# Performance work log

Hardware: AMD Instinct MI355X
Metric: run time of the kernel (lower is better)

Reference implementation:

```python
import jax, jax.numpy as jnp
import numpy as np

NEG_SLOPE = 0.2  # PyG GATConv default negative_slope
EPS = 1e-16      # PyG softmax denominator epsilon


def gat_conv(x, src, dst, W, b, att_src, att_dst, num_nodes):
    """PyG GATConv, heads=1, add_self_loops=True (self loops already in src/dst).
    x: [N, Fin]; src/dst: [E]; W: [Fin, Fout]; att_src/att_dst: [Fout]."""
    h = x @ W                                  # [N, Fout]
    a_src = h @ att_src                        # [N]
    a_dst = h @ att_dst                        # [N]
    e = jax.nn.leaky_relu(a_src[src] + a_dst[dst], NEG_SLOPE)  # [E]
    m = jax.ops.segment_max(e, dst, num_segments=num_nodes)    # softmax over edges grouped by dst
    ex = jnp.exp(e - m[dst])
    denom = jax.ops.segment_sum(ex, dst, num_segments=num_nodes)
    alpha = ex / (denom[dst] + EPS)            # [E]
    out = jax.ops.segment_sum(alpha[:, None] * h[src], dst, num_segments=num_nodes)
    return out + b


def global_attention(x, gate_w, gate_b):
    """PyG GlobalAttention with a single graph: softmax(gate_nn(x)) weighted sum."""
    gate = x @ gate_w + gate_b                 # [N, 1]
    attn = jax.nn.softmax(gate, axis=0)        # softmax over all nodes (one graph)
    return jnp.sum(attn * x, axis=0, keepdims=True)  # [1, F]


def setup_inputs() -> dict:
    key = jax.random.key(0)
    ks = jax.random.split(key, 12)
    N, E, D, H = 50000, 800000, 768, 256
    x = jax.random.normal(ks[0], (N, D), dtype=jnp.float32)
    edge_index = jax.random.randint(ks[1], (2, E), 0, N, dtype=jnp.int64)
    s = 1.0 / np.sqrt(D)
    W1 = jax.random.normal(ks[2], (D, H), dtype=jnp.float32) * s
    b1 = jnp.zeros((H,), dtype=jnp.float32)
    as1 = jax.random.normal(ks[3], (H,), dtype=jnp.float32) * (1.0 / np.sqrt(H))
    ad1 = jax.random.normal(ks[4], (H,), dtype=jnp.float32) * (1.0 / np.sqrt(H))
    s2 = 1.0 / np.sqrt(H)
    W2 = jax.random.normal(ks[5], (H, H), dtype=jnp.float32) * s2
    b2 = jnp.zeros((H,), dtype=jnp.float32)
    as2 = jax.random.normal(ks[6], (H,), dtype=jnp.float32) * s2
    ad2 = jax.random.normal(ks[7], (H,), dtype=jnp.float32) * s2
    gate_w = jax.random.normal(ks[8], (H, 1), dtype=jnp.float32) * s2
    gate_b = jnp.zeros((1,), dtype=jnp.float32)
    return {"x": x, "edge_index": edge_index, "W1": W1, "b1": b1, "as1": as1,
            "ad1": ad1, "W2": W2, "b2": b2, "as2": as2, "ad2": ad2,
            "gate_w": gate_w, "gate_b": gate_b}


def reference(x, edge_index, W1, b1, as1, ad1, W2, b2, as2, ad2, gate_w, gate_b):
    N = x.shape[0]
    loops = jnp.arange(N, dtype=edge_index.dtype)
    src = jnp.concatenate([edge_index[0], loops])  # add self loops (GATConv default)
    dst = jnp.concatenate([edge_index[1], loops])
    h = gat_conv(x, src, dst, W1, b1, as1, ad1, N)
    h = jax.nn.relu(h)
    h = gat_conv(h, src, dst, W2, b2, as2, ad2, N)
    h = jax.nn.relu(h)
    return global_attention(h, gate_w, gate_b)   # [1, 256]
```

## Files before the change

### kernel.cpp

```cpp
#include <hip/hip_runtime.h>

#define WAVE 64
#define LRELU(x) ((x) > 0.0f ? (x) : 0.2f * (x))

typedef __attribute__((ext_vector_type(8))) short bf16x8;
typedef __attribute__((ext_vector_type(4))) float f32x4;

__device__ __forceinline__ void gld16(const void* g, void* l) {
    __builtin_amdgcn_global_load_lds((const __attribute__((address_space(1))) unsigned int*)g,
                                     (__attribute__((address_space(3))) unsigned int*)l,
                                     16, 0, 0);
}

__device__ __forceinline__ unsigned short f2bf_hi(float f) {
    unsigned u = __builtin_bit_cast(unsigned, f);
    u += 0x7FFF + ((u >> 16) & 1);
    return (unsigned short)(u >> 16);
}

__device__ __forceinline__ float4 bf4_to_f32(ushort4 v) {
    float4 r;
    r.x = __builtin_bit_cast(float, (unsigned)v.x << 16);
    r.y = __builtin_bit_cast(float, (unsigned)v.y << 16);
    r.z = __builtin_bit_cast(float, (unsigned)v.z << 16);
    r.w = __builtin_bit_cast(float, (unsigned)v.w << 16);
    return r;
}

__device__ __forceinline__ void split8(f32x4 a, f32x4 b, bf16x8& hi, bf16x8& lo) {
    float f[8] = {a[0], a[1], a[2], a[3], b[0], b[1], b[2], b[3]};
#pragma unroll
    for (int e = 0; e < 8; e++) {
        unsigned u = __builtin_bit_cast(unsigned, f[e]);
        float hf = __builtin_bit_cast(float, u & 0xFFFF0000u);
        float fl = f[e] - hf;
        unsigned u2 = __builtin_bit_cast(unsigned, fl);
        unsigned t2 = u2 + 0x7FFF + ((u2 >> 16) & 1);
        hi[e] = (short)(u >> 16);
        lo[e] = (short)(t2 >> 16);
    }
}

__global__ __launch_bounds__(256) void k_gemm_f32A(const float* __restrict__ A,
                                                   const unsigned short* __restrict__ Bh,
                                                   const unsigned short* __restrict__ Bl,
                                                   unsigned short* __restrict__ Cb,
                                                   float* __restrict__ asrc,
                                                   float* __restrict__ adst,
                                                   const float* __restrict__ att_s,
                                                   const float* __restrict__ att_d,
                                                   int M, int K) {
    __shared__ char smem[32768];
    char* SAH = smem;
    char* SAL = smem + 8192;
    char* SBH = smem + 16384;
    char* SBL = smem + 24576;

    const int tid = threadIdx.x, lane = tid & 63, w = tid >> 6;
    const int m16 = lane & 15, q = lane >> 4;
    const int row0 = blockIdx.x * 128, col0 = blockIdx.y * 128;

    f32x4 acc[4][4];
#pragma unroll
    for (int i = 0; i < 4; i++)
#pragma unroll
        for (int j = 0; j < 4; j++) acc[i][j] = (f32x4){0.f, 0.f, 0.f, 0.f};

    const int s_row = tid >> 1;
    const int s_mt  = s_row >> 4, s_m16 = s_row & 15;
    const int s_q0  = (tid & 1) * 2;
    int s_grow = row0 + s_row;
    if (s_grow > M - 1) s_grow = M - 1;
    const f32x4* aptr = (const f32x4*)&A[(size_t)s_grow * K] + (tid & 1) * 4;
    const int s_off = (s_mt * 4 + s_q0) * 256 + s_m16 * 16;

    const int b_rloc = lane >> 2;
    const int b_kb   = (lane & 3) * 16;

    f32x4 pre0 = aptr[0], pre1 = aptr[1], pre2 = aptr[2], pre3 = aptr[3];

    for (int k0 = 0; k0 < K; k0 += 32) {
#pragma unroll
        for (int s = 0; s < 2; s++) {
            int c = w * 2 + s;
            int brow = col0 + c * 16 + b_rloc;
            gld16((const char*)Bh + ((size_t)brow * K + k0) * 2 + b_kb, SBH + c * 1024);
            gld16((const char*)Bl + ((size_t)brow * K + k0) * 2 + b_kb, SBL + c * 1024);
        }
        {
            bf16x8 h0, l0, h1, l1;
            split8(pre0, pre1, h0, l0);
            split8(pre2, pre3, h1, l1);
            *(bf16x8*)(SAH + s_off)       = h0;
            *(bf16x8*)(SAL + s_off)       = l0;
            *(bf16x8*)(SAH + s_off + 256) = h1;
            *(bf16x8*)(SAL + s_off + 256) = l1;
        }
        __syncthreads();

        if (k0 + 32 < K) {
            aptr += 8;
            pre0 = aptr[0]; pre1 = aptr[1]; pre2 = aptr[2]; pre3 = aptr[3];
        }

        bf16x8 bh[4], bl[4];
#pragma unroll
        for (int nt = 0; nt < 4; nt++) {
            int r = (w & 1) * 64 + nt * 16 + m16;
            bh[nt] = *(bf16x8*)(SBH + r * 64 + q * 16);
            bl[nt] = *(bf16x8*)(SBL + r * 64 + q * 16);
        }
#pragma unroll
        for (int mt = 0; mt < 4; mt++) {
            int frag = ((w >> 1) * 4 + mt) * 4 + q;
            bf16x8 ah = *(bf16x8*)(SAH + frag * 256 + m16 * 16);
            bf16x8 al = *(bf16x8*)(SAL + frag * 256 + m16 * 16);
#pragma unroll
            for (int nt = 0; nt < 4; nt++) {
                acc[mt][nt] = __builtin_amdgcn_mfma_f32_16x16x32_bf16(ah, bh[nt], acc[mt][nt], 0, 0, 0);
                acc[mt][nt] = __builtin_amdgcn_mfma_f32_16x16x32_bf16(ah, bl[nt], acc[mt][nt], 0, 0, 0);
                acc[mt][nt] = __builtin_amdgcn_mfma_f32_16x16x32_bf16(al, bh[nt], acc[mt][nt], 0, 0, 0);
            }
        }
        __syncthreads();
    }

    const int rbase = row0 + (w >> 1) * 64;
    const int cbase = col0 + (w & 1) * 64;
#pragma unroll
    for (int mt = 0; mt < 4; mt++)
#pragma unroll
        for (int r = 0; r < 4; r++) {
            int row = rbase + mt * 16 + q * 4 + r;
            if (row < M) {
#pragma unroll
                for (int nt = 0; nt < 4; nt++)
                    Cb[(size_t)row * 256 + cbase + nt * 16 + m16] = f2bf_hi(acc[mt][nt][r]);
            }
        }
    float as_v[4], ad_v[4];
#pragma unroll
    for (int nt = 0; nt < 4; nt++) {
        as_v[nt] = att_s[cbase + nt * 16 + m16];
        ad_v[nt] = att_d[cbase + nt * 16 + m16];
    }
#pragma unroll
    for (int mt = 0; mt < 4; mt++)
#pragma unroll
        for (int r = 0; r < 4; r++) {
            float s = 0.f, d = 0.f;
#pragma unroll
            for (int nt = 0; nt < 4; nt++) {
                float v = acc[mt][nt][r];
                s = fmaf(v, as_v[nt], s);
                d = fmaf(v, ad_v[nt], d);
            }
#pragma unroll
            for (int off = 1; off < 16; off <<= 1) {
                s += __shfl_xor(s, off);
                d += __shfl_xor(d, off);
            }
            int row = rbase + mt * 16 + q * 4 + r;
            if (m16 == 0 && row < M) {
                atomicAdd(&asrc[row], s);
                atomicAdd(&adst[row], d);
            }
        }
}

__global__ __launch_bounds__(256) void k_gemm_bf16A(const unsigned short* __restrict__ Ah,
                                                    const unsigned short* __restrict__ Al,
                                                    const unsigned short* __restrict__ Bh,
                                                    const unsigned short* __restrict__ Bl,
                                                    unsigned short* __restrict__ Cb,
                                                    float* __restrict__ asrc,
                                                    float* __restrict__ adst,
                                                    const float* __restrict__ att_s,
                                                    const float* __restrict__ att_d,
                                                    int M, int K) {
    __shared__ char smem[32768];
    char* SAH = smem;
    char* SAL = smem + 8192;
    char* SBH = smem + 16384;
    char* SBL = smem + 24576;

    const int tid = threadIdx.x, lane = tid & 63, w = tid >> 6;
    const int m16 = lane & 15, q = lane >> 4;
    const int row0 = blockIdx.x * 128, col0 = blockIdx.y * 128;

    f32x4 acc[4][4];
#pragma unroll
    for (int i = 0; i < 4; i++)
#pragma unroll
        for (int j = 0; j < 4; j++) acc[i][j] = (f32x4){0.f, 0.f, 0.f, 0.f};

    const int rloc = lane >> 2;
    const int kb   = (lane & 3) * 16;

    for (int k0 = 0; k0 < K; k0 += 32) {
#pragma unroll
        for (int s = 0; s < 2; s++) {
            int c = w * 2 + s;
            int arow = row0 + c * 16 + rloc;
            int brow = col0 + c * 16 + rloc;
            gld16((const char*)Ah + ((size_t)arow * K + k0) * 2 + kb, SAH + c * 1024);
            gld16((const char*)Al + ((size_t)arow * K + k0) * 2 + kb, SAL + c * 1024);
            gld16((const char*)Bh + ((size_t)brow * K + k0) * 2 + kb, SBH + c * 1024);
            gld16((const char*)Bl + ((size_t)brow * K + k0) * 2 + kb, SBL + c * 1024);
        }
        __syncthreads();

        bf16x8 bh[4], bl[4];
#pragma unroll
        for (int nt = 0; nt < 4; nt++) {
            int r = (w & 1) * 64 + nt * 16 + m16;
            bh[nt] = *(bf16x8*)(SBH + r * 64 + q * 16);
            bl[nt] = *(bf16x8*)(SBL + r * 64 + q * 16);
        }
#pragma unroll
        for (int mt = 0; mt < 4; mt++) {
            int r = (w >> 1) * 64 + mt * 16 + m16;
            bf16x8 ah = *(bf16x8*)(SAH + r * 64 + q * 16);
            bf16x8 al = *(bf16x8*)(SAL + r * 64 + q * 16);
#pragma unroll
            for (int nt = 0; nt < 4; nt++) {
                acc[mt][nt] = __builtin_amdgcn_mfma_f32_16x16x32_bf16(ah, bh[nt], acc[mt][nt], 0, 0, 0);
                acc[mt][nt] = __builtin_amdgcn_mfma_f32_16x16x32_bf16(ah, bl[nt], acc[mt][nt], 0, 0, 0);
                acc[mt][nt] = __builtin_amdgcn_mfma_f32_16x16x32_bf16(al, bh[nt], acc[mt][nt], 0, 0, 0);
            }
        }
        __syncthreads();
    }

    const int rbase = row0 + (w >> 1) * 64;
    const int cbase = col0 + (w & 1) * 64;
#pragma unroll
    for (int mt = 0; mt < 4; mt++)
#pragma unroll
        for (int r = 0; r < 4; r++) {
            int row = rbase + mt * 16 + q * 4 + r;
            if (row < M) {
#pragma unroll
                for (int nt = 0; nt < 4; nt++)
                    Cb[(size_t)row * 256 + cbase + nt * 16 + m16] = f2bf_hi(acc[mt][nt][r]);
            }
        }
    float as_v[4], ad_v[4];
#pragma unroll
    for (int nt = 0; nt < 4; nt++) {
        as_v[nt] = att_s[cbase + nt * 16 + m16];
        ad_v[nt] = att_d[cbase + nt * 16 + m16];
    }
#pragma unroll
    for (int mt = 0; mt < 4; mt++)
#pragma unroll
        for (int r = 0; r < 4; r++) {
            float s = 0.f, d = 0.f;
#pragma unroll
            for (int nt = 0; nt < 4; nt++) {
                float v = acc[mt][nt][r];
                s = fmaf(v, as_v[nt], s);
                d = fmaf(v, ad_v[nt], d);
            }
#pragma unroll
            for (int off = 1; off < 16; off <<= 1) {
                s += __shfl_xor(s, off);
                d += __shfl_xor(d, off);
            }
            int row = rbase + mt * 16 + q * 4 + r;
            if (m16 == 0 && row < M) {
                atomicAdd(&asrc[row], s);
                atomicAdd(&adst[row], d);
            }
        }
}

__global__ __launch_bounds__(256) void k_convB(const float* __restrict__ W,
                                               unsigned short* __restrict__ BThi,
                                               unsigned short* __restrict__ BTlo, int K) {
    int idx = blockIdx.x * 256 + threadIdx.x;
    int k = idx >> 8, n = idx & 255;
    if (k >= K) return;
    float f = W[(size_t)k * 256 + n];
    unsigned u = __builtin_bit_cast(unsigned, f);
    unsigned t = u + 0x7FFF + ((u >> 16) & 1);
    float hf = __builtin_bit_cast(float, t & 0xFFFF0000u);
    unsigned short lb = f2bf_hi(f - hf);
    BThi[(size_t)n * K + k] = (unsigned short)(t >> 16);
    BTlo[(size_t)n * K + k] = lb;
}

__global__ __launch_bounds__(256) void k_degree(const int* __restrict__ dst,
                                                int* __restrict__ counts, int E) {
    int e = blockIdx.x * 256 + threadIdx.x;
    if (e < E) atomicAdd(&counts[dst[e]], 1);
}

__global__ __launch_bounds__(256) void k_part(const int* __restrict__ counts,
                                              int* __restrict__ psum, int N) {
    __shared__ int red[256];
    int tid = threadIdx.x;
    int i = blockIdx.x * 256 + tid;
    red[tid] = (i < N) ? counts[i] : 0;
    __syncthreads();
    for (int off = 128; off; off >>= 1) {
        if (tid < off) red[tid] += red[tid + off];
        __syncthreads();
    }
    if (tid == 0) psum[blockIdx.x] = red[0];
}

__global__ __launch_bounds__(256) void k_scan_part(int* __restrict__ psum, int nb,
                                                   int* __restrict__ total_out) {
    __shared__ int s[256];
    int tid = threadIdx.x;
    int v = (tid < nb) ? psum[tid] : 0;
    s[tid] = v;
    __syncthreads();
    for (int off = 1; off < 256; off <<= 1) {
        int t = (tid >= off) ? s[tid - off] : 0;
        __syncthreads();
        s[tid] += t;
        __syncthreads();
    }
    if (tid < nb) psum[tid] = s[tid] - v;
    if (tid == 255) *total_out = s[255];
}

__global__ __launch_bounds__(256) void k_rowptr(const int* __restrict__ counts,
                                                const int* __restrict__ psum,
                                                int* __restrict__ rowptr,
                                                int* __restrict__ cursor, int N) {
    __shared__ int s[256];
    int tid = threadIdx.x;
    int i = blockIdx.x * 256 + tid;
    int v = (i < N) ? counts[i] : 0;
    s[tid] = v;
    __syncthreads();
    for (int off = 1; off < 256; off <<= 1) {
        int t = (tid >= off) ? s[tid - off] : 0;
        __syncthreads();
        s[tid] += t;
        __syncthreads();
    }
    if (i < N) {
        int excl = psum[blockIdx.x] + s[tid] - v;
        rowptr[i] = excl;
        cursor[i] = excl;
    }
}

__global__ __launch_bounds__(256) void k_scatter(const int* __restrict__ src,
                                                 const int* __restrict__ dst,
                                                 int* __restrict__ cursor,
                                                 int* __restrict__ col, int E) {
    int e = blockIdx.x * 256 + threadIdx.x;
    if (e < E) {
        int p = atomicAdd(&cursor[dst[e]], 1);
        col[p] = src[e];
    }
}

__global__ __launch_bounds__(256) void k_edge(const unsigned short* __restrict__ hb,
                                              const float* __restrict__ asrc,
                                              const float* __restrict__ adst,
                                              const int* __restrict__ rowptr,
                                              const int* __restrict__ col,
                                              const float* __restrict__ bias,
                                              float* __restrict__ outf,
                                              unsigned short* __restrict__ outh,
                                              unsigned short* __restrict__ outl,
                                              const float* __restrict__ gw,
                                              const float* __restrict__ gb,
                                              float* __restrict__ gatep, int N) {
    int wid = threadIdx.x >> 6;
    int lane = threadIdx.x & 63;
    int node = blockIdx.x * 4 + wid;
    if (node >= N) return;
    int start = rowptr[node], end = rowptr[node + 1];
    float ad = adst[node];
    float eself = asrc[node] + ad;
    eself = LRELU(eself);
    float m = eself;
    for (int j = start + lane; j < end; j += WAVE) {
        float e = asrc[col[j]] + ad;
        e = LRELU(e);
        m = fmaxf(m, e);
    }
#pragma unroll
    for (int off = 32; off; off >>= 1) m = fmaxf(m, __shfl_xor(m, off));

    float wself = __expf(eself - m);
    float denom = wself;
    float4 hv = bf4_to_f32(*(const ushort4*)&hb[(size_t)node * 256 + lane * 4]);
    float ax = wself * hv.x, ay = wself * hv.y, az = wself * hv.z, aw = wself * hv.w;
    int j = start;
    for (; j + 4 <= end; j += 4) {
        int s0 = col[j], s1 = col[j + 1], s2 = col[j + 2], s3 = col[j + 3];
        float w0 = __expf(LRELU(asrc[s0] + ad) - m);
        float w1 = __expf(LRELU(asrc[s1] + ad) - m);
        float w2 = __expf(LRELU(asrc[s2] + ad) - m);
        float w3 = __expf(LRELU(asrc[s3] + ad) - m);
        denom += w0 + w1 + w2 + w3;
        float4 h0 = bf4_to_f32(*(const ushort4*)&hb[(size_t)s0 * 256 + lane * 4]);
        float4 h1 = bf4_to_f32(*(const ushort4*)&hb[(size_t)s1 * 256 + lane * 4]);
        float4 h2 = bf4_to_f32(*(const ushort4*)&hb[(size_t)s2 * 256 + lane * 4]);
        float4 h3 = bf4_to_f32(*(const ushort4*)&hb[(size_t)s3 * 256 + lane * 4]);
        ax = fmaf(w0, h0.x, fmaf(w1, h1.x, fmaf(w2, h2.x, fmaf(w3, h3.x, ax))));
        ay = fmaf(w0, h0.y, fmaf(w1, h1.y, fmaf(w2, h2.y, fmaf(w3, h3.y, ay))));
        az = fmaf(w0, h0.z, fmaf(w1, h1.z, fmaf(w2, h2.z, fmaf(w3, h3.z, az))));
        aw = fmaf(w0, h0.w, fmaf(w1, h1.w, fmaf(w2, h2.w, fmaf(w3, h3.w, aw))));
    }
    for (; j < end; j++) {
        int s = col[j];
        float wgt = __expf(LRELU(asrc[s] + ad) - m);
        denom += wgt;
        float4 hx = bf4_to_f32(*(const ushort4*)&hb[(size_t)s * 256 + lane * 4]);
        ax = fmaf(wgt, hx.x, ax); ay = fmaf(wgt, hx.y, ay);
        az = fmaf(wgt, hx.z, az); aw = fmaf(wgt, hx.w, aw);
    }
    float inv = 1.0f / (denom + 1e-16f);
    float4 bv = *(const float4*)&bias[lane * 4];
    float ox = fmaxf(fmaf(ax, inv, bv.x), 0.0f);
    float oy = fmaxf(fmaf(ay, inv, bv.y), 0.0f);
    float oz = fmaxf(fmaf(az, inv, bv.z), 0.0f);
    float ow = fmaxf(fmaf(aw, inv, bv.w), 0.0f);
    if (outf) {
        float4 o = make_float4(ox, oy, oz, ow);
        *(float4*)&outf[(size_t)node * 256 + lane * 4] = o;
    }
    if (outh) {
        float of[4] = {ox, oy, oz, ow};
        unsigned long long ph = 0, pl = 0;
#pragma unroll
        for (int e = 0; e < 4; e++) {
            unsigned u = __builtin_bit_cast(unsigned, of[e]);
            unsigned t = u + 0x7FFF + ((u >> 16) & 1);
            float hf = __builtin_bit_cast(float, t & 0xFFFF0000u);
            float fl = of[e] - hf;
            unsigned u2 = __builtin_bit_cast(unsigned, fl);
            unsigned t2 = u2 + 0x7FFF + ((u2 >> 16) & 1);
            ph |= ((unsigned long long)(t >> 16)) << (16 * e);
            pl |= ((unsigned long long)(t2 >> 16)) << (16 * e);
        }
        *(unsigned long long*)&outh[(size_t)node * 256 + lane * 4] = ph;
        *(unsigned long long*)&outl[(size_t)node * 256 + lane * 4] = pl;
    }
    if (gatep) {
        float4 gv = *(const float4*)&gw[lane * 4];
        float s = ox * gv.x + oy * gv.y + oz * gv.z + ow * gv.w;
#pragma unroll
        for (int off = 32; off; off >>= 1) s += __shfl_xor(s, off);
        if (lane == 0) gatep[node] = s + gb[0];
    }
}

__global__ __launch_bounds__(256) void k_pmax(const float* __restrict__ gate, int N,
                                              float* __restrict__ pmax) {
    __shared__ float red[256];
    int tid = threadIdx.x;
    float m = -3.0e38f;
    for (int i = blockIdx.x * 256 + tid; i < N; i += gridDim.x * 256) m = fmaxf(m, gate[i]);
    red[tid] = m;
    __syncthreads();
    for (int off = 128; off; off >>= 1) {
        if (tid < off) red[tid] = fmaxf(red[tid], red[tid + off]);
        __syncthreads();
    }
    if (tid == 0) pmax[blockIdx.x] = red[0];
}

__global__ __launch_bounds__(256) void k_gmid(const float* __restrict__ pmax, int nb,
                                              float* __restrict__ scal,
                                              float* __restrict__ gout) {
    __shared__ float red[256];
    int tid = threadIdx.x;
    red[tid] = (tid < nb) ? pmax[tid] : -3.0e38f;
    __syncthreads();
    for (int off = 128; off; off >>= 1) {
        if (tid < off) red[tid] = fmaxf(red[tid], red[tid + off]);
        __syncthreads();
    }
    if (tid == 0) { scal[0] = red[0]; scal[1] = 0.0f; }
    gout[tid] = 0.0f;
}

__global__ __launch_bounds__(256) void k_gout(const float* __restrict__ h,
                                              const float* __restrict__ gate,
                                              float* __restrict__ scal_rw,
                                              float* __restrict__ gout, int N) {
    int f = threadIdx.x;
    float gmax = scal_rw[0];
    float acc = 0.0f, sumw = 0.0f;
    for (int i = blockIdx.x; i < N; i += gridDim.x) {
        float w = __expf(gate[i] - gmax);
        acc = fmaf(w, h[(size_t)i * 256 + f], acc);
        sumw += w;
    }
    atomicAdd(&gout[f], acc);
    if (f == 0) atomicAdd(&scal_rw[1], sumw);
}

__global__ __launch_bounds__(256) void k_final(const float* __restrict__ gout,
                                               const float* __restrict__ scal,
                                               float* __restrict__ out) {
    int f = threadIdx.x;
    out[f] = gout[f] / scal[1];
}

extern "C" void kernel_launch(void* const* d_in, const int* in_sizes, int n_in,
                              void* d_out, int out_size, void* d_ws, size_t ws_size,
                              hipStream_t stream) {
    const float* x   = (const float*)d_in[0];
    const int*   ei  = (const int*)d_in[1];
    const float* W1  = (const float*)d_in[2];
    const float* b1  = (const float*)d_in[3];
    const float* as1 = (const float*)d_in[4];
    const float* ad1 = (const float*)d_in[5];
    const float* W2  = (const float*)d_in[6];
    const float* b2  = (const float*)d_in[7];
    const float* as2 = (const float*)d_in[8];
    const float* ad2 = (const float*)d_in[9];
    const float* gw  = (const float*)d_in[10];
    const float* gb  = (const float*)d_in[11];
    float* out = (float*)d_out;

    const int N = in_sizes[0] / 768;
    const int E = in_sizes[1] / 2;
    const int Mpad = (N + 127) & ~127;
    const int* srcA = ei;
    const int* dstA = ei + E;

    char* w = (char*)d_ws;
    auto alloc = [&](size_t bytes) -> void* {
        void* p = (void*)w;
        w += (bytes + 255) & ~(size_t)255;
        return p;
    };
    unsigned short* bufHb = (unsigned short*)alloc((size_t)N * 256 * 2);
    unsigned short* X2h = (unsigned short*)alloc((size_t)Mpad * 256 * 2);
    unsigned short* X2l = (unsigned short*)alloc((size_t)Mpad * 256 * 2);
    float* bufX = (float*)X2h;
    float* asrc   = (float*)alloc((size_t)N * 4);
    float* adst   = (float*)alloc((size_t)N * 4);
    float* gate   = (float*)alloc((size_t)N * 4);
    int*   counts = (int*)alloc((size_t)N * 4);
    int*   rowptr = (int*)alloc((size_t)(N + 1) * 4);
    int*   cursor = (int*)alloc((size_t)N * 4);
    int*   colbuf = (int*)alloc((size_t)E * 4);
    int*   psum   = (int*)alloc(256 * 4);
    float* pmax   = (float*)alloc(256 * 4);
    float* scal   = (float*)alloc(8 * 4);
    float* gout   = (float*)alloc(256 * 4);
    unsigned short* BT1h = (unsigned short*)alloc((size_t)256 * 768 * 2);
    unsigned short* BT1l = (unsigned short*)alloc((size_t)256 * 768 * 2);
    unsigned short* BT2h = (unsigned short*)alloc((size_t)256 * 256 * 2);
    unsigned short* BT2l = (unsigned short*)alloc((size_t)256 * 256 * 2);

    const int eb  = (E + 255) / 256;
    const int nb4 = (N + 3) / 4;
    const int nb  = (N + 255) / 256;
    const dim3 gg(Mpad / 128, 2);

    k_convB<<<768, 256, 0, stream>>>(W1, BT1h, BT1l, 768);
    k_convB<<<256, 256, 0, stream>>>(W2, BT2h, BT2l, 256);

    (void)hipMemsetAsync(counts, 0, (size_t)N * 4, stream);
    k_degree<<<eb, 256, 0, stream>>>(dstA, counts, E);
    k_part<<<nb, 256, 0, stream>>>(counts, psum, N);
    k_scan_part<<<1, 256, 0, stream>>>(psum, nb, rowptr + N);
    k_rowptr<<<nb, 256, 0, stream>>>(counts, psum, rowptr, cursor, N);
    k_scatter<<<eb, 256, 0, stream>>>(srcA, dstA, cursor, colbuf, E);

    (void)hipMemsetAsync(asrc, 0, (size_t)N * 4, stream);
    (void)hipMemsetAsync(adst, 0, (size_t)N * 4, stream);
    k_gemm_f32A<<<gg, 256, 0, stream>>>(x, BT1h, BT1l, bufHb, asrc, adst, as1, ad1, N, 768);
    k_edge<<<nb4, 256, 0, stream>>>(bufHb, asrc, adst, rowptr, colbuf, b1,
                                    nullptr, X2h, X2l, nullptr, nullptr, nullptr, N);

    (void)hipMemsetAsync(asrc, 0, (size_t)N * 4, stream);
    (void)hipMemsetAsync(adst, 0, (size_t)N * 4, stream);
    k_gemm_bf16A<<<gg, 256, 0, stream>>>(X2h, X2l, BT2h, BT2l, bufHb, asrc, adst, as2, ad2, N, 256);
    k_edge<<<nb4, 256, 0, stream>>>(bufHb, asrc, adst, rowptr, colbuf, b2,
                                    bufX, nullptr, nullptr, gw, gb, gate, N);

    k_pmax<<<64, 256, 0, stream>>>(gate, N, pmax);
    k_gmid<<<1, 256, 0, stream>>>(pmax, 64, scal, gout);
    k_gout<<<256, 256, 0, stream>>>(bufX, gate, scal, gout, N);
    k_final<<<1, 256, 0, stream>>>(gout, scal, out);
}
```

Baseline: 629.9 us.

## Replace per-node softmax max pass with global max bound; double-buffer GEMM B tiles

The edge kernel no longer scans each node's neighbours to find the segment max. It uses an upper bound, LRELU(global max of asrc + adst[node]), computed by a new pmax+fold reduction, which removes one gather pass over the edges. The main aggregation loop is also unrolled from 4 to 8 neighbours to expose more memory-level parallelism. The f32-A GEMM double-buffers B tiles in shared memory and prefetches A two stages ahead. The risk is exp underflow when a node's true max is far below the bound, which makes the result less numerically robust, plus two extra small launches per layer.

```diff
diff --git a/kernel.cpp b/kernel.cpp
--- a/kernel.cpp
+++ b/kernel.cpp
@@ -50,11 +50,11 @@
                                                    const float* __restrict__ att_s,
                                                    const float* __restrict__ att_d,
                                                    int M, int K) {
-    __shared__ char smem[32768];
+    __shared__ char smem[49152];
     char* SAH = smem;
     char* SAL = smem + 8192;
-    char* SBH = smem + 16384;
-    char* SBL = smem + 24576;
+    char* SB0 = smem + 16384;
+    char* SB1 = smem + 32768;
 
     const int tid = threadIdx.x, lane = tid & 63, w = tid >> 6;
     const int m16 = lane & 15, q = lane >> 4;
@@ -77,38 +77,37 @@
     const int b_rloc = lane >> 2;
     const int b_kb   = (lane & 3) * 16;
 
-    f32x4 pre0 = aptr[0], pre1 = aptr[1], pre2 = aptr[2], pre3 = aptr[3];
-
-    for (int k0 = 0; k0 < K; k0 += 32) {
+    f32x4 r0[4], r1[4];
+
+    auto stageB = [&](int k0, char* SB) {
 #pragma unroll
         for (int s = 0; s < 2; s++) {
             int c = w * 2 + s;
             int brow = col0 + c * 16 + b_rloc;
-            gld16((const char*)Bh + ((size_t)brow * K + k0) * 2 + b_kb, SBH + c * 1024);
-            gld16((const char*)Bl + ((size_t)brow * K + k0) * 2 + b_kb, SBL + c * 1024);
-        }
-        {
-            bf16x8 h0, l0, h1, l1;
-            split8(pre0, pre1, h0, l0);
-            split8(pre2, pre3, h1, l1);
-            *(bf16x8*)(SAH + s_off)       = h0;
-            *(bf16x8*)(SAL + s_off)       = l0;
-            *(bf16x8*)(SAH + s_off + 256) = h1;
-            *(bf16x8*)(SAL + s_off + 256) = l1;
-        }
-        __syncthreads();
-
-        if (k0 + 32 < K) {
-            aptr += 8;
-            pre0 = aptr[0]; pre1 = aptr[1]; pre2 = aptr[2]; pre3 = aptr[3];
-        }
-
+            gld16((const char*)Bh + ((size_t)brow * K + k0) * 2 + b_kb, SB + c * 1024);
+            gld16((const char*)Bl + ((size_t)brow * K + k0) * 2 + b_kb, SB + 8192 + c * 1024);
+        }
+    };
+    auto loadA = [&](f32x4* r) {
+        r[0] = aptr[0]; r[1] = aptr[1]; r[2] = aptr[2]; r[3] = aptr[3];
+        aptr += 8;
+    };
+    auto splitA = [&](f32x4* r) {
+        bf16x8 h0, l0, h1, l1;
+        split8(r[0], r[1], h0, l0);
+        split8(r[2], r[3], h1, l1);
+        *(bf16x8*)(SAH + s_off)       = h0;
+        *(bf16x8*)(SAL + s_off)       = l0;
+        *(bf16x8*)(SAH + s_off + 256) = h1;
+        *(bf16x8*)(SAL + s_off + 256) = l1;
+    };
+    auto mfma = [&](char* SB) {
         bf16x8 bh[4], bl[4];
 #pragma unroll
         for (int nt = 0; nt < 4; nt++) {
             int r = (w & 1) * 64 + nt * 16 + m16;
-            bh[nt] = *(bf16x8*)(SBH + r * 64 + q * 16);
-            bl[nt] = *(bf16x8*)(SBL + r * 64 + q * 16);
+            bh[nt] = *(bf16x8*)(SB + r * 64 + q * 16);
+            bl[nt] = *(bf16x8*)(SB + 8192 + r * 64 + q * 16);
         }
 #pragma unroll
         for (int mt = 0; mt < 4; mt++) {
@@ -122,7 +121,32 @@
                 acc[mt][nt] = __builtin_amdgcn_mfma_f32_16x16x32_bf16(al, bh[nt], acc[mt][nt], 0, 0, 0);
             }
         }
-        __syncthreads();
+    };
+
+    const int iters = K / 32;
+    loadA(r0);
+    stageB(0, SB0);
+    splitA(r0);
+    loadA(r1);
+    __syncthreads();
+
+    for (int i = 0; i < iters; i += 2) {
+        if (i + 1 < iters) stageB((i + 1) * 32, SB1);
+        if (i + 2 < iters) loadA(r0);
+        mfma(SB0);
+        __syncthreads();
+        if (i + 1 < iters) {
+            splitA(r1);
+            __syncthreads();
+            if (i + 2 < iters) stageB((i + 2) * 32, SB0);
+            if (i + 3 < iters) loadA(r1);
+            mfma(SB1);
+            __syncthreads();
+            if (i + 2 < iters) {
+                splitA(r0);
+                __syncthreads();
+            }
+        }
     }
 
     const int rbase = row0 + (w >> 1) * 64;
@@ -364,6 +388,7 @@
 __global__ __launch_bounds__(256) void k_edge(const unsigned short* __restrict__ hb,
                                               const float* __restrict__ asrc,
                                               const float* __restrict__ adst,
+                                              const float* __restrict__ gmaxv,
                                               const int* __restrict__ rowptr,
                                               const int* __restrict__ col,
                                               const float* __restrict__ bias,
@@ -377,39 +402,44 @@
     int lane = threadIdx.x & 63;
     int node = blockIdx.x * 4 + wid;
     if (node >= N) return;
-    int start = rowptr[node], end = rowptr[node + 1];
+    int j = rowptr[node], end = rowptr[node + 1];
     float ad = adst[node];
-    float eself = asrc[node] + ad;
-    eself = LRELU(eself);
-    float m = eself;
-    for (int j = start + lane; j < end; j += WAVE) {
-        float e = asrc[col[j]] + ad;
-        e = LRELU(e);
-        m = fmaxf(m, e);
-    }
-#pragma unroll
-    for (int off = 32; off; off >>= 1) m = fmaxf(m, __shfl_xor(m, off));
-
-    float wself = __expf(eself - m);
+    float gm = gmaxv[0] + ad;
+    float m = LRELU(gm);
+
+    float wself = __expf(LRELU(asrc[node] + ad) - m);
     float denom = wself;
     float4 hv = bf4_to_f32(*(const ushort4*)&hb[(size_t)node * 256 + lane * 4]);
     float ax = wself * hv.x, ay = wself * hv.y, az = wself * hv.z, aw = wself * hv.w;
-    int j = start;
-    for (; j + 4 <= end; j += 4) {
-        int s0 = col[j], s1 = col[j + 1], s2 = col[j + 2], s3 = col[j + 3];
+
+    for (; j + 8 <= end; j += 8) {
+        int s0 = col[j], s1 = col[j+1], s2 = col[j+2], s3 = col[j+3];
+        int s4 = col[j+4], s5 = col[j+5], s6 = col[j+6], s7 = col[j+7];
         float w0 = __expf(LRELU(asrc[s0] + ad) - m);
         float w1 = __expf(LRELU(asrc[s1] + ad) - m);
         float w2 = __expf(LRELU(asrc[s2] + ad) - m);
         float w3 = __expf(LRELU(asrc[s3] + ad) - m);
-        denom += w0 + w1 + w2 + w3;
+        float w4 = __expf(LRELU(asrc[s4] + ad) - m);
+        float w5 = __expf(LRELU(asrc[s5] + ad) - m);
+        float w6 = __expf(LRELU(asrc[s6] + ad) - m);
+        float w7 = __expf(LRELU(asrc[s7] + ad) - m);
+        denom += w0 + w1 + w2 + w3 + w4 + w5 + w6 + w7;
         float4 h0 = bf4_to_f32(*(const ushort4*)&hb[(size_t)s0 * 256 + lane * 4]);
         float4 h1 = bf4_to_f32(*(const ushort4*)&hb[(size_t)s1 * 256 + lane * 4]);
         float4 h2 = bf4_to_f32(*(const ushort4*)&hb[(size_t)s2 * 256 + lane * 4]);
         float4 h3 = bf4_to_f32(*(const ushort4*)&hb[(size_t)s3 * 256 + lane * 4]);
-        ax = fmaf(w0, h0.x, fmaf(w1, h1.x, fmaf(w2, h2.x, fmaf(w3, h3.x, ax))));
-        ay = fmaf(w0, h0.y, fmaf(w1, h1.y, fmaf(w2, h2.y, fmaf(w3, h3.y, ay))));
-        az = fmaf(w0, h0.z, fmaf(w1, h1.z, fmaf(w2, h2.z, fmaf(w3, h3.z, az))));
-        aw = fmaf(w0, h0.w, fmaf(w1, h1.w, fmaf(w2, h2.w, fmaf(w3, h3.w, aw))));
+        float4 h4 = bf4_to_f32(*(const ushort4*)&hb[(size_t)s4 * 256 + lane * 4]);
+        float4 h5 = bf4_to_f32(*(const ushort4*)&hb[(size_t)s5 * 256 + lane * 4]);
+        float4 h6 = bf4_to_f32(*(const ushort4*)&hb[(size_t)s6 * 256 + lane * 4]);
+        float4 h7 = bf4_to_f32(*(const ushort4*)&hb[(size_t)s7 * 256 + lane * 4]);
+        ax = fmaf(w0,h0.x, fmaf(w1,h1.x, fmaf(w2,h2.x, fmaf(w3,h3.x,
+             fmaf(w4,h4.x, fmaf(w5,h5.x, fmaf(w6,h6.x, fmaf(w7,h7.x, ax))))))));
+        ay = fmaf(w0,h0.y, fmaf(w1,h1.y, fmaf(w2,h2.y, fmaf(w3,h3.y,
+             fmaf(w4,h4.y, fmaf(w5,h5.y, fmaf(w6,h6.y, fmaf(w7,h7.y, ay))))))));
+        az = fmaf(w0,h0.z, fmaf(w1,h1.z, fmaf(w2,h2.z, fmaf(w3,h3.z,
+             fmaf(w4,h4.z, fmaf(w5,h5.z, fmaf(w6,h6.z, fmaf(w7,h7.z, az))))))));
+        aw = fmaf(w0,h0.w, fmaf(w1,h1.w, fmaf(w2,h2.w, fmaf(w3,h3.w,
+             fmaf(w4,h4.w, fmaf(w5,h5.w, fmaf(w6,h6.w, fmaf(w7,h7.w, aw))))))));
     }
     for (; j < end; j++) {
         int s = col[j];
@@ -455,12 +485,12 @@
     }
 }
 
-__global__ __launch_bounds__(256) void k_pmax(const float* __restrict__ gate, int N,
+__global__ __launch_bounds__(256) void k_pmax(const float* __restrict__ v, int N,
                                               float* __restrict__ pmax) {
     __shared__ float red[256];
     int tid = threadIdx.x;
     float m = -3.0e38f;
-    for (int i = blockIdx.x * 256 + tid; i < N; i += gridDim.x * 256) m = fmaxf(m, gate[i]);
+    for (int i = blockIdx.x * 256 + tid; i < N; i += gridDim.x * 256) m = fmaxf(m, v[i]);
     red[tid] = m;
     __syncthreads();
     for (int off = 128; off; off >>= 1) {
@@ -468,6 +498,15 @@
         __syncthreads();
     }
     if (tid == 0) pmax[blockIdx.x] = red[0];
+}
+
+__global__ __launch_bounds__(64) void k_fold(const float* __restrict__ p,
+                                             float* __restrict__ o) {
+    int lane = threadIdx.x;
+    float m = p[lane];
+#pragma unroll
+    for (int off = 32; off; off >>= 1) m = fmaxf(m, __shfl_xor(m, off));
+    if (lane == 0) o[0] = m;
 }
 
 __global__ __launch_bounds__(256) void k_gmid(const float* __restrict__ pmax, int nb,
@@ -550,6 +589,7 @@
     int*   colbuf = (int*)alloc((size_t)E * 4);
     int*   psum   = (int*)alloc(256 * 4);
     float* pmax   = (float*)alloc(256 * 4);
+    float* gmaxv  = (float*)alloc(4 * 4);
     float* scal   = (float*)alloc(8 * 4);
     float* gout   = (float*)alloc(256 * 4);
     unsigned short* BT1h = (unsigned short*)alloc((size_t)256 * 768 * 2);
@@ -575,13 +615,17 @@
     (void)hipMemsetAsync(asrc, 0, (size_t)N * 4, stream);
     (void)hipMemsetAsync(adst, 0, (size_t)N * 4, stream);
     k_gemm_f32A<<<gg, 256, 0, stream>>>(x, BT1h, BT1l, bufHb, asrc, adst, as1, ad1, N, 768);
-    k_edge<<<nb4, 256, 0, stream>>>(bufHb, asrc, adst, rowptr, colbuf, b1,
+    k_pmax<<<64, 256, 0, stream>>>(asrc, N, pmax);
+    k_fold<<<1, 64, 0, stream>>>(pmax, gmaxv);
+    k_edge<<<nb4, 256, 0, stream>>>(bufHb, asrc, adst, gmaxv, rowptr, colbuf, b1,
                                     nullptr, X2h, X2l, nullptr, nullptr, nullptr, N);
 
     (void)hipMemsetAsync(asrc, 0, (size_t)N * 4, stream);
     (void)hipMemsetAsync(adst, 0, (size_t)N * 4, stream);
     k_gemm_bf16A<<<gg, 256, 0, stream>>>(X2h, X2l, BT2h, BT2l, bufHb, asrc, adst, as2, ad2, N, 256);
-    k_edge<<<nb4, 256, 0, stream>>>(bufHb, asrc, adst, rowptr, colbuf, b2,
+    k_pmax<<<64, 256, 0, stream>>>(asrc, N, pmax);
+    k_fold<<<1, 64, 0, stream>>>(pmax, gmaxv);
+    k_edge<<<nb4, 256, 0, stream>>>(bufHb, asrc, adst, gmaxv, rowptr, colbuf, b2,
                                     bufX, nullptr, nullptr, gw, gb, gate, N);
 
     k_pmax<<<64, 256, 0, stream>>>(gate, N, pmax);
```

Measured after the change: 643.4 us. 2.1% more time.

## Use global asrc max as softmax shift and half-wave 16B gathers in edge kernel

Applied to the files above, without the earlier changes.

The per-destination max pass over each node's edges is replaced by a shared upper bound, leaky_relu(max(asrc) + adst[node]). Softmax is invariant to the shift and leaky_relu is monotonic, so the result is unchanged, and the extra pass that gathers asrc[col] for every edge goes away. The global max comes from a new k_pmax plus k_fold pair launched before each edge kernel. The edge kernel now gives each node a half-wave, with each lane loading 8 bf16 values as one 16-byte vector, so each block covers 8 nodes. The risk is exp underflow for nodes whose scores sit far below the global maximum, and the change adds two small kernel launches per layer.

```diff
diff --git a/kernel.cpp b/kernel.cpp
--- a/kernel.cpp
+++ b/kernel.cpp
@@ -4,6 +4,7 @@
 #define LRELU(x) ((x) > 0.0f ? (x) : 0.2f * (x))
 
 typedef __attribute__((ext_vector_type(8))) short bf16x8;
+typedef __attribute__((ext_vector_type(8))) unsigned short u16x8;
 typedef __attribute__((ext_vector_type(4))) float f32x4;
 
 __device__ __forceinline__ void gld16(const void* g, void* l) {
@@ -16,15 +17,6 @@
     unsigned u = __builtin_bit_cast(unsigned, f);
     u += 0x7FFF + ((u >> 16) & 1);
     return (unsigned short)(u >> 16);
-}
-
-__device__ __forceinline__ float4 bf4_to_f32(ushort4 v) {
-    float4 r;
-    r.x = __builtin_bit_cast(float, (unsigned)v.x << 16);
-    r.y = __builtin_bit_cast(float, (unsigned)v.y << 16);
-    r.z = __builtin_bit_cast(float, (unsigned)v.z << 16);
-    r.w = __builtin_bit_cast(float, (unsigned)v.w << 16);
-    return r;
 }
 
 __device__ __forceinline__ void split8(f32x4 a, f32x4 b, bf16x8& hi, bf16x8& lo) {
@@ -364,6 +356,7 @@
 __global__ __launch_bounds__(256) void k_edge(const unsigned short* __restrict__ hb,
                                               const float* __restrict__ asrc,
                                               const float* __restrict__ adst,
+                                              const float* __restrict__ gmaxv,
                                               const int* __restrict__ rowptr,
                                               const int* __restrict__ col,
                                               const float* __restrict__ bias,
@@ -373,94 +366,102 @@
                                               const float* __restrict__ gw,
                                               const float* __restrict__ gb,
                                               float* __restrict__ gatep, int N) {
-    int wid = threadIdx.x >> 6;
-    int lane = threadIdx.x & 63;
-    int node = blockIdx.x * 4 + wid;
+    int hw = threadIdx.x >> 5;
+    int l  = threadIdx.x & 31;
+    int node = blockIdx.x * 8 + hw;
     if (node >= N) return;
-    int start = rowptr[node], end = rowptr[node + 1];
+    int j = rowptr[node], end = rowptr[node + 1];
     float ad = adst[node];
-    float eself = asrc[node] + ad;
-    eself = LRELU(eself);
-    float m = eself;
-    for (int j = start + lane; j < end; j += WAVE) {
-        float e = asrc[col[j]] + ad;
-        e = LRELU(e);
-        m = fmaxf(m, e);
-    }
-#pragma unroll
-    for (int off = 32; off; off >>= 1) m = fmaxf(m, __shfl_xor(m, off));
-
-    float wself = __expf(eself - m);
-    float denom = wself;
-    float4 hv = bf4_to_f32(*(const ushort4*)&hb[(size_t)node * 256 + lane * 4]);
-    float ax = wself * hv.x, ay = wself * hv.y, az = wself * hv.z, aw = wself * hv.w;
-    int j = start;
-    for (; j + 4 <= end; j += 4) {
-        int s0 = col[j], s1 = col[j + 1], s2 = col[j + 2], s3 = col[j + 3];
-        float w0 = __expf(LRELU(asrc[s0] + ad) - m);
-        float w1 = __expf(LRELU(asrc[s1] + ad) - m);
-        float w2 = __expf(LRELU(asrc[s2] + ad) - m);
-        float w3 = __expf(LRELU(asrc[s3] + ad) - m);
-        denom += w0 + w1 + w2 + w3;
-        float4 h0 = bf4_to_f32(*(const ushort4*)&hb[(size_t)s0 * 256 + lane * 4]);
-        float4 h1 = bf4_to_f32(*(const ushort4*)&hb[(size_t)s1 * 256 + lane * 4]);
-        float4 h2 = bf4_to_f32(*(const ushort4*)&hb[(size_t)s2 * 256 + lane * 4]);
-        float4 h3 = bf4_to_f32(*(const ushort4*)&hb[(size_t)s3 * 256 + lane * 4]);
-        ax = fmaf(w0, h0.x, fmaf(w1, h1.x, fmaf(w2, h2.x, fmaf(w3, h3.x, ax))));
-        ay = fmaf(w0, h0.y, fmaf(w1, h1.y, fmaf(w2, h2.y, fmaf(w3, h3.y, ay))));
-        az = fmaf(w0, h0.z, fmaf(w1, h1.z, fmaf(w2, h2.z, fmaf(w3, h3.z, az))));
-        aw = fmaf(w0, h0.w, fmaf(w1, h1.w, fmaf(w2, h2.w, fmaf(w3, h3.w, aw))));
-    }
-    for (; j < end; j++) {
-        int s = col[j];
-        float wgt = __expf(LRELU(asrc[s] + ad) - m);
-        denom += wgt;
-        float4 hx = bf4_to_f32(*(const ushort4*)&hb[(size_t)s * 256 + lane * 4]);
-        ax = fmaf(wgt, hx.x, ax); ay = fmaf(wgt, hx.y, ay);
-        az = fmaf(wgt, hx.z, az); aw = fmaf(wgt, hx.w, aw);
-    }
-    float inv = 1.0f / (denom + 1e-16f);
-    float4 bv = *(const float4*)&bias[lane * 4];
-    float ox = fmaxf(fmaf(ax, inv, bv.x), 0.0f);
-    float oy = fmaxf(fmaf(ay, inv, bv.y), 0.0f);
-    float oz = fmaxf(fmaf(az, inv, bv.z), 0.0f);
-    float ow = fmaxf(fmaf(aw, inv, bv.w), 0.0f);
+    float m = LRELU(gmaxv[0] + ad);
+
+    float a[8];
+    {
+        float wself = __expf(LRELU(asrc[node] + ad) - m);
+        u16x8 hv = *(const u16x8*)&hb[(size_t)node * 256 + l * 8];
+#pragma unroll
+        for (int e = 0; e < 8; e++)
+            a[e] = wself * __builtin_bit_cast(float, (unsigned)hv[e] << 16);
+        float denom = wself;
+
+        for (; j + 4 <= end; j += 4) {
+            int s0 = col[j], s1 = col[j + 1], s2 = col[j + 2], s3 = col[j + 3];
+            float w0 = __expf(LRELU(asrc[s0] + ad) - m);
+            float w1 = __expf(LRELU(asrc[s1] + ad) - m);
+            float w2 = __expf(LRELU(asrc[s2] + ad) - m);
+            float w3 = __expf(LRELU(asrc[s3] + ad) - m);
+            denom += w0 + w1 + w2 + w3;
+            u16x8 h0 = *(const u16x8*)&hb[(size_t)s0 * 256 + l * 8];
+            u16x8 h1 = *(const u16x8*)&hb[(size_t)s1 * 256 + l * 8];
+            u16x8 h2 = *(const u16x8*)&hb[(size_t)s2 * 256 + l * 8];
+            u16x8 h3 = *(const u16x8*)&hb[(size_t)s3 * 256 + l * 8];
+#pragma unroll
+            for (int e = 0; e < 8; e++) {
+                float f0 = __builtin_bit_cast(float, (unsigned)h0[e] << 16);
+                float f1 = __builtin_bit_cast(float, (unsigned)h1[e] << 16);
+                float f2 = __builtin_bit_cast(float, (unsigned)h2[e] << 16);
+                float f3 = __builtin_bit_cast(float, (unsigned)h3[e] << 16);
+                a[e] = fmaf(w0, f0, fmaf(w1, f1, fmaf(w2, f2, fmaf(w3, f3, a[e]))));
+            }
+        }
+        for (; j < end; j++) {
+            int s = col[j];
+            float wgt = __expf(LRELU(asrc[s] + ad) - m);
+            denom += wgt;
+            u16x8 hx = *(const u16x8*)&hb[(size_t)s * 256 + l * 8];
+#pragma unroll
+            for (int e = 0; e < 8; e++)
+                a[e] = fmaf(wgt, __builtin_bit_cast(float, (unsigned)hx[e] << 16), a[e]);
+        }
+        float inv = 1.0f / (denom + 1e-16f);
+#pragma unroll
+        for (int e = 0; e < 8; e++) a[e] *= inv;
+    }
+
+    float o[8];
+    {
+        float4 bv0 = *(const float4*)&bias[l * 8];
+        float4 bv1 = *(const float4*)&bias[l * 8 + 4];
+        float bb[8] = {bv0.x, bv0.y, bv0.z, bv0.w, bv1.x, bv1.y, bv1.z, bv1.w};
+#pragma unroll
+        for (int e = 0; e < 8; e++) o[e] = fmaxf(a[e] + bb[e], 0.0f);
+    }
     if (outf) {
-        float4 o = make_float4(ox, oy, oz, ow);
-        *(float4*)&outf[(size_t)node * 256 + lane * 4] = o;
+        float4 o0 = make_float4(o[0], o[1], o[2], o[3]);
+        float4 o1 = make_float4(o[4], o[5], o[6], o[7]);
+        *(float4*)&outf[(size_t)node * 256 + l * 8]     = o0;
+        *(float4*)&outf[(size_t)node * 256 + l * 8 + 4] = o1;
     }
     if (outh) {
-        float of[4] = {ox, oy, oz, ow};
-        unsigned long long ph = 0, pl = 0;
-#pragma unroll
-        for (int e = 0; e < 4; e++) {
-            unsigned u = __builtin_bit_cast(unsigned, of[e]);
-            unsigned t = u + 0x7FFF + ((u >> 16) & 1);
-            float hf = __builtin_bit_cast(float, t & 0xFFFF0000u);
-            float fl = of[e] - hf;
+        u16x8 ph, pl;
+#pragma unroll
+        for (int e = 0; e < 8; e++) {
+            unsigned u = __builtin_bit_cast(unsigned, o[e]);
+            float hf = __builtin_bit_cast(float, u & 0xFFFF0000u);
+            float fl = o[e] - hf;
             unsigned u2 = __builtin_bit_cast(unsigned, fl);
             unsigned t2 = u2 + 0x7FFF + ((u2 >> 16) & 1);
-            ph |= ((unsigned long long)(t >> 16)) << (16 * e);
-            pl |= ((unsigned long long)(t2 >> 16)) << (16 * e);
-        }
-        *(unsigned long long*)&outh[(size_t)node * 256 + lane * 4] = ph;
-        *(unsigned long long*)&outl[(size_t)node * 256 + lane * 4] = pl;
+            ph[e] = (unsigned short)(u >> 16);
+            pl[e] = (unsigned short)(t2 >> 16);
+        }
+        *(u16x8*)&outh[(size_t)node * 256 + l * 8] = ph;
+        *(u16x8*)&outl[(size_t)node * 256 + l * 8] = pl;
     }
     if (gatep) {
-        float4 gv = *(const float4*)&gw[lane * 4];
-        float s = ox * gv.x + oy * gv.y + oz * gv.z + ow * gv.w;
-#pragma unroll
-        for (int off = 32; off; off >>= 1) s += __shfl_xor(s, off);
-        if (lane == 0) gatep[node] = s + gb[0];
-    }
-}
-
-__global__ __launch_bounds__(256) void k_pmax(const float* __restrict__ gate, int N,
+        float s = 0.f;
+#pragma unroll
+        for (int e = 0; e < 8; e++) s = fmaf(o[e], gw[l * 8 + e], s);
+#pragma unroll
+        for (int off = 16; off; off >>= 1) s += __shfl_xor(s, off);
+        if (l == 0) gatep[node] = s + gb[0];
+    }
+}
+
+__global__ __launch_bounds__(256) void k_pmax(const float* __restrict__ v, int N,
                                               float* __restrict__ pmax) {
     __shared__ float red[256];
     int tid = threadIdx.x;
     float m = -3.0e38f;
-    for (int i = blockIdx.x * 256 + tid; i < N; i += gridDim.x * 256) m = fmaxf(m, gate[i]);
+    for (int i = blockIdx.x * 256 + tid; i < N; i += gridDim.x * 256) m = fmaxf(m, v[i]);
     red[tid] = m;
     __syncthreads();
     for (int off = 128; off; off >>= 1) {
@@ -468,6 +469,15 @@
         __syncthreads();
     }
     if (tid == 0) pmax[blockIdx.x] = red[0];
+}
+
+__global__ __launch_bounds__(64) void k_fold(const float* __restrict__ p,
+                                             float* __restrict__ o) {
+    int lane = threadIdx.x;
+    float m = p[lane];
+#pragma unroll
+    for (int off = 32; off; off >>= 1) m = fmaxf(m, __shfl_xor(m, off));
+    if (lane == 0) o[0] = m;
 }
 
 __global__ __launch_bounds__(256) void k_gmid(const float* __restrict__ pmax, int nb,
@@ -550,6 +560,7 @@
     int*   colbuf = (int*)alloc((size_t)E * 4);
     int*   psum   = (int*)alloc(256 * 4);
     float* pmax   = (float*)alloc(256 * 4);
+    float* gmaxv  = (float*)alloc(4 * 4);
     float* scal   = (float*)alloc(8 * 4);
     float* gout   = (float*)alloc(256 * 4);
     unsigned short* BT1h = (unsigned short*)alloc((size_t)256 * 768 * 2);
@@ -558,7 +569,7 @@
     unsigned short* BT2l = (unsigned short*)alloc((size_t)256 * 256 * 2);
 
     const int eb  = (E + 255) / 256;
-    const int nb4 = (N + 3) / 4;
+    const int nb8 = (N + 7) / 8;
     const int nb  = (N + 255) / 256;
     const dim3 gg(Mpad / 128, 2);
 
@@ -575,13 +586,17 @@
     (void)hipMemsetAsync(asrc, 0, (size_t)N * 4, stream);
     (void)hipMemsetAsync(adst, 0, (size_t)N * 4, stream);
     k_gemm_f32A<<<gg, 256, 0, stream>>>(x, BT1h, BT1l, bufHb, asrc, adst, as1, ad1, N, 768);
-    k_edge<<<nb4, 256, 0, stream>>>(bufHb, asrc, adst, rowptr, colbuf, b1,
+    k_pmax<<<64, 256, 0, stream>>>(asrc, N, pmax);
+    k_fold<<<1, 64, 0, stream>>>(pmax, gmaxv);
+    k_edge<<<nb8, 256, 0, stream>>>(bufHb, asrc, adst, gmaxv, rowptr, colbuf, b1,
                                     nullptr, X2h, X2l, nullptr, nullptr, nullptr, N);
 
     (void)hipMemsetAsync(asrc, 0, (size_t)N * 4, stream);
     (void)hipMemsetAsync(adst, 0, (size_t)N * 4, stream);
     k_gemm_bf16A<<<gg, 256, 0, stream>>>(X2h, X2l, BT2h, BT2l, bufHb, asrc, adst, as2, ad2, N, 256);
-    k_edge<<<nb4, 256, 0, stream>>>(bufHb, asrc, adst, rowptr, colbuf, b2,
+    k_pmax<<<64, 256, 0, stream>>>(asrc, N, pmax);
+    k_fold<<<1, 64, 0, stream>>>(pmax, gmaxv);
+    k_edge<<<nb8, 256, 0, stream>>>(bufHb, asrc, adst, gmaxv, rowptr, colbuf, b2,
                                     bufX, nullptr, nullptr, gw, gb, gate, N);
 
     k_pmax<<<64, 256, 0, stream>>>(gate, N, pmax);
```

Result: no change. 635.0 us (+0.8%).
